# Optimization experiments

Hardware: AMD Instinct MI355X
Metric: run time of the kernel (lower is better)

The kernel has to match this reference:

```python
import jax, jax.numpy as jnp
import numpy as np

EPS = 1e-5

def _layernorm(x, g, b):
    mu = jnp.mean(x, axis=-1, keepdims=True)
    var = jnp.mean((x - mu) ** 2, axis=-1, keepdims=True)
    return (x - mu) / jnp.sqrt(var + EPS) * g + b


def setup_inputs() -> dict:
    key = jax.random.key(0)
    ks = jax.random.split(key, 4)
    B, H, W, C = 8, 96, 96, 256
    return {
        "x1": jax.random.normal(ks[0], (B, H, W, C), dtype=jnp.float32),
        "x2": jax.random.normal(ks[1], (B, H, W, C), dtype=jnp.float32),
        # norm1 (shared LayerNorm applied to both x1 and x2)
        "g1": jnp.ones((C,), jnp.float32),
        "b1": jnp.zeros((C,), jnp.float32),
        # reprojection 1x1 conv: C -> 2C
        "Wr": jax.random.normal(ks[2], (2 * C, C), dtype=jnp.float32) * 0.05,
        "br": jnp.zeros((2 * C,), jnp.float32),
        # final LayerNorm over 2C
        "g2": jnp.ones((2 * C,), jnp.float32),
        "b2": jnp.zeros((2 * C,), jnp.float32),
        # learnable mixing scalars
        "a1": jnp.array(0.25, jnp.float32),
        "a2": jnp.array(0.25, jnp.float32),
        "a3": jnp.array(0.25, jnp.float32),
        "a4": jnp.array(0.25, jnpp_ := jnp.float32),
    }


def reference(x1, x2, g1, b1, Wr, br, g2, b2, a1, a2, a3, a4):
    B, H, W, C = x1.shape
    N, D = H * W, C  # head_count = 1, key_channels = value_channels = D
    n1 = _layernorm(x1.reshape(B, N, C), g1, b1)  # [B,N,D]
    n2 = _layernorm(x2.reshape(B, N, C), g1, b1)

    kq = jnp.swapaxes(n2, 1, 2)                   # [B,D,N]
    key_sm = jax.nn.softmax(kq, axis=2)           # softmax over N
    query = jax.nn.softmax(kq, axis=1)            # softmax over D
    value = jnp.swapaxes(n1, 1, 2)                # [B,D,N]

    # context = key @ value^T : [B,D,D]
    context = jnp.einsum('bdn,ben->bde', key_sm, value)

    def masked_softmax(k):
        # torch.topk + scatter mask == keep entries >= k-th largest per row
        thr = jax.lax.top_k(context, k)[0][..., -1:]
        return jax.nn.softmax(jnp.where(context >= thr, context, -jnp.inf), axis=-1)

    ks = [D // 2, (D * 2) // 3, (D * 3) // 4, (D * 4) // 5]
    o = [jnp.einsum('bde,ben->bdn', masked_softmax(k), query) for k in ks]
    att = a1 * o[0] + a2 * o[1] + a3 * o[2] + a4 * o[3]  # [B,D,N]

    # 1x1 conv reprojection D -> 2D, then LayerNorm over channels
    rep = jnp.einsum('oc,bcn->bno', Wr, att) + br         # [B,N,2D]
    rep = _layernorm(rep, g2, b2)
    # view(B,H,W,2C).permute(0,3,1,2)
    return jnp.transpose(rep.reshape(B, H, W, 2 * C), (0, 3, 1, 2))
```

## Files before the change

### kernel.cpp

```cpp
#include <hip/hip_runtime.h>
#include <hip/hip_bf16.h>

#define Bc 8
#define Nn 9216
#define Dd 256
#define Oo 512
#define EPSc 1e-5f

#define OFF_MU1    0
#define OFF_RSTD1  73728
#define OFF_MU2    147456
#define OFF_RSTD2  221184
#define OFF_ROWINV 294912
#define OFF_COLSUM 368640
#define OFF_M      894976
#define OFF_W2T    1419264
#define OFF_CTXP   2467840

typedef __attribute__((ext_vector_type(4))) float f32x4;
typedef __attribute__((ext_vector_type(8))) short short8;
typedef __attribute__((ext_vector_type(8))) unsigned short ushort8;

static __device__ __forceinline__ unsigned short f2bf(float f) {
    __hip_bfloat16 h = __float2bfloat16(f);
    union { __hip_bfloat16 hh; unsigned short uu; } cv; cv.hh = h;
    return cv.uu;
}

#define SWZ(ch) (((((ch) >> 2) & 7)) ^ ((((ch) & 3)) << 1))

__global__ __launch_bounds__(256) void mg_k0_zero(float* __restrict__ p, int n4) {
    int i = blockIdx.x * 256 + threadIdx.x;
    if (i < n4) ((float4*)p)[i] = make_float4(0.f, 0.f, 0.f, 0.f);
}

__global__ __launch_bounds__(256) void mg_k1_stats(const float* __restrict__ x1, const float* __restrict__ x2,
                                                   const float* __restrict__ g1, const float* __restrict__ b1,
                                                   float* __restrict__ ws)
{
    float* mu1    = ws + OFF_MU1;
    float* rstd1  = ws + OFF_RSTD1;
    float* mu2    = ws + OFF_MU2;
    float* rstd2  = ws + OFF_RSTD2;
    float* rowinv = ws + OFF_ROWINV;
    float* colsum = ws + OFF_COLSUM;

    int t = threadIdx.x, lane = t & 63, w = t >> 6;
    int b = blockIdx.x / 144, rb = blockIdx.x % 144;
    int nbase = rb * 64;

    float4 g1v = ((const float4*)g1)[lane];
    float4 b1v = ((const float4*)b1)[lane];
    float cs0 = 0.f, cs1 = 0.f, cs2 = 0.f, cs3 = 0.f;
    __shared__ float csL[4][256];

    for (int i = 0; i < 16; ++i) {
        int n = nbase + i * 4 + w;
        int base = (b * Nn + n) * 64 + lane;
        float4 xa = ((const float4*)x1)[base];
        float4 xb = ((const float4*)x2)[base];
        float s1 = xa.x + xa.y + xa.z + xa.w;
        float q1 = xa.x*xa.x + xa.y*xa.y + xa.z*xa.z + xa.w*xa.w;
        float s2 = xb.x + xb.y + xb.z + xb.w;
        float q2 = xb.x*xb.x + xb.y*xb.y + xb.z*xb.z + xb.w*xb.w;
        #pragma unroll
        for (int m = 1; m < 64; m <<= 1) {
            s1 += __shfl_xor(s1, m); q1 += __shfl_xor(q1, m);
            s2 += __shfl_xor(s2, m); q2 += __shfl_xor(q2, m);
        }
        float m1 = s1 * (1.f / Dd), m2 = s2 * (1.f / Dd);
        float r1 = rsqrtf(q1 * (1.f / Dd) - m1 * m1 + EPSc);
        float r2 = rsqrtf(q2 * (1.f / Dd) - m2 * m2 + EPSc);
        int ni = b * Nn + n;
        if (lane == 0) { mu1[ni] = m1; rstd1[ni] = r1; mu2[ni] = m2; rstd2[ni] = r2; }
        float e0 = __expf((xb.x - m2) * r2 * g1v.x + b1v.x);
        float e1 = __expf((xb.y - m2) * r2 * g1v.y + b1v.y);
        float e2 = __expf((xb.z - m2) * r2 * g1v.z + b1v.z);
        float e3 = __expf((xb.w - m2) * r2 * g1v.w + b1v.w);
        float rs = e0 + e1 + e2 + e3;
        #pragma unroll
        for (int m = 1; m < 64; m <<= 1) rs += __shfl_xor(rs, m);
        if (lane == 0) rowinv[ni] = 1.f / rs;
        cs0 += e0; cs1 += e1; cs2 += e2; cs3 += e3;
    }
    csL[w][lane * 4 + 0] = cs0;
    csL[w][lane * 4 + 1] = cs1;
    csL[w][lane * 4 + 2] = cs2;
    csL[w][lane * 4 + 3] = cs3;
    __syncthreads();
    float tot = csL[0][t] + csL[1][t] + csL[2][t] + csL[3][t];
    atomicAdd(&colsum[b * Dd + t], tot);
}

__global__ __launch_bounds__(512, 2) void mg_k3_ctx(const float* __restrict__ x1, const float* __restrict__ x2,
                                                    const float* __restrict__ g1, const float* __restrict__ b1,
                                                    float* __restrict__ ws, int nks)
{
    __shared__ ushort PA[256 * 64];
    __shared__ ushort PB[256 * 64];
    const float* mu1   = ws + OFF_MU1;
    const float* rstd1 = ws + OFF_RSTD1;
    const float* mu2   = ws + OFF_MU2;
    const float* rstd2 = ws + OFF_RSTD2;
    float* ctxp = ws + OFF_CTXP;

    int t = threadIdx.x;
    int ks_i = blockIdx.x % nks;
    int b = blockIdx.x / nks;
    int krange = Nn / nks;
    int ntiles = krange >> 6;
    int n_base = ks_i * krange;

    int o  = t >> 6;
    int c4 = t & 63;

    f32x4 g1v = ((const f32x4*)g1)[c4];
    f32x4 b1v = ((const f32x4*)b1)[c4];

    int lane = t & 63, wave = t >> 6;
    int wd = wave & 3, we = wave >> 2;
    int l15 = lane & 15, kgrp = lane >> 4;

    f32x4 acc[4][8];
    #pragma unroll
    for (int dt = 0; dt < 4; ++dt)
        #pragma unroll
        for (int et = 0; et < 8; ++et) acc[dt][et] = (f32x4){0.f, 0.f, 0.f, 0.f};

    for (int st = 0; st < ntiles; ++st) {
        int rowb = b * Nn + n_base + st * 64 + o * 8;
        __syncthreads();
        {
            f32x4 mv0 = *(const f32x4*)(mu1 + rowb),   mv1 = *(const f32x4*)(mu1 + rowb + 4);
            f32x4 rv0 = *(const f32x4*)(rstd1 + rowb), rv1 = *(const f32x4*)(rstd1 + rowb + 4);
            float mva[8] = {mv0[0], mv0[1], mv0[2], mv0[3], mv1[0], mv1[1], mv1[2], mv1[3]};
            float rva[8] = {rv0[0], rv0[1], rv0[2], rv0[3], rv1[0], rv1[1], rv1[2], rv1[3]};
            f32x4 xv[8];
            #pragma unroll
            for (int rr = 0; rr < 8; ++rr)
                xv[rr] = ((const f32x4*)x1)[(size_t)(rowb + rr) * 64 + c4];
            #pragma unroll
            for (int i = 0; i < 4; ++i) {
                int ch = c4 * 4 + i;
                ushort8 u;
                #pragma unroll
                for (int rr = 0; rr < 8; ++rr)
                    u[rr] = f2bf((xv[rr][i] - mva[rr]) * rva[rr] * g1v[i] + b1v[i]);
                *(ushort8*)&PB[ch * 64 + ((o + SWZ(ch)) & 7) * 8] = u;
            }
        }
        {
            f32x4 mv0 = *(const f32x4*)(mu2 + rowb),   mv1 = *(const f32x4*)(mu2 + rowb + 4);
            f32x4 rv0 = *(const f32x4*)(rstd2 + rowb), rv1 = *(const f32x4*)(rstd2 + rowb + 4);
            float mva[8] = {mv0[0], mv0[1], mv0[2], mv0[3], mv1[0], mv1[1], mv1[2], mv1[3]};
            float rva[8] = {rv0[0], rv0[1], rv0[2], rv0[3], rv1[0], rv1[1], rv1[2], rv1[3]};
            f32x4 xv[8];
            #pragma unroll
            for (int rr = 0; rr < 8; ++rr)
                xv[rr] = ((const f32x4*)x2)[(size_t)(rowb + rr) * 64 + c4];
            #pragma unroll
            for (int i = 0; i < 4; ++i) {
                int ch = c4 * 4 + i;
                ushort8 u;
                #pragma unroll
                for (int rr = 0; rr < 8; ++rr)
                    u[rr] = f2bf(__expf((xv[rr][i] - mva[rr]) * rva[rr] * g1v[i] + b1v[i]));
                *(ushort8*)&PA[ch * 64 + ((o + SWZ(ch)) & 7) * 8] = u;
            }
        }
        __syncthreads();

        #pragma unroll
        for (int kk = 0; kk < 2; ++kk) {
            short8 af[4], bf[8];
            #pragma unroll
            for (int dt = 0; dt < 4; ++dt) {
                int ch = wd * 64 + dt * 16 + l15;
                af[dt] = *(const short8*)&PA[ch * 64 + (((kk << 2) + kgrp + SWZ(ch)) & 7) * 8];
            }
            #pragma unroll
            for (int et = 0; et < 8; ++et) {
                int ch = we * 128 + et * 16 + l15;
                bf[et] = *(const short8*)&PB[ch * 64 + (((kk << 2) + kgrp + SWZ(ch)) & 7) * 8];
            }
            #pragma unroll
            for (int dt = 0; dt < 4; ++dt)
                #pragma unroll
                for (int et = 0; et < 8; ++et)
                    acc[dt][et] = __builtin_amdgcn_mfma_f32_16x16x32_bf16(af[dt], bf[et], acc[dt][et], 0, 0, 0);
        }
    }

    size_t obase = ((size_t)ks_i * Bc + b) * (Dd * Dd);
    #pragma unroll
    for (int dt = 0; dt < 4; ++dt) {
        #pragma unroll
        for (int r = 0; r < 4; ++r) {
            int d = wd * 64 + dt * 16 + kgrp * 4 + r;
            float* rowp = ctxp + obase + (size_t)d * Dd + we * 128 + l15;
            #pragma unroll
            for (int et = 0; et < 8; ++et)
                rowp[et * 16] = acc[dt][et][r];
        }
    }
}

__global__ __launch_bounds__(256) void mg_k5_mask(const float* __restrict__ a1p, const float* __restrict__ a2p,
                                                  const float* __restrict__ a3p, const float* __restrict__ a4p,
                                                  float* __restrict__ ws, int nks)
{
    const float* ctxp   = ws + OFF_CTXP;
    const float* colsum = ws + OFF_COLSUM;
    float* Mo = ws + OFF_M;
    int t = threadIdx.x;
    int b = blockIdx.x >> 8, d = blockIdx.x & 255;
    __shared__ float s[256];
    __shared__ float wred[4][4];

    float c = 0.f;
    for (int p = 0; p < nks; ++p)
        c += ctxp[((size_t)p * Bc + b) * (Dd * Dd) + (size_t)d * Dd + t];
    float inv = 1.f / colsum[b * Dd + d];
    c *= inv;
    s[t] = c;
    __syncthreads();
    for (int k = 2; k <= 256; k <<= 1) {
        for (int j = k >> 1; j > 0; j >>= 1) {
            int ixj = t ^ j;
            if (ixj > t) {
                float A = s[t], Bv = s[ixj];
                bool desc = ((t & k) == 0);
                bool sw = desc ? (A < Bv) : (A > Bv);
                if (sw) { s[t] = Bv; s[ixj] = A; }
            }
            __syncthreads();
        }
    }
    float cmax = s[0];
    float t0 = s[127], t1 = s[169], t2 = s[191], t3 = s[203];
    float e = __expf(c - cmax);
    float w0 = (c >= t0) ? e : 0.f;
    float w1 = (c >= t1) ? e : 0.f;
    float w2 = (c >= t2) ? e : 0.f;
    float w3 = (c >= t3) ? e : 0.f;
    float v0 = w0, v1 = w1, v2 = w2, v3 = w3;
    #pragma unroll
    for (int m = 1; m < 64; m <<= 1) {
        v0 += __shfl_xor(v0, m); v1 += __shfl_xor(v1, m);
        v2 += __shfl_xor(v2, m); v3 += __shfl_xor(v3, m);
    }
    int lane = t & 63, wv = t >> 6;
    if (lane == 0) { wred[wv][0] = v0; wred[wv][1] = v1; wred[wv][2] = v2; wred[wv][3] = v3; }
    __syncthreads();
    float S0 = wred[0][0] + wred[1][0] + wred[2][0] + wred[3][0];
    float S1 = wred[0][1] + wred[1][1] + wred[2][1] + wred[3][1];
    float S2 = wred[0][2] + wred[1][2] + wred[2][2] + wred[3][2];
    float S3 = wred[0][3] + wred[1][3] + wred[2][3] + wred[3][3];
    float Mv = a1p[0] * (w0 / S0) + a2p[0] * (w1 / S1) + a3p[0] * (w2 / S2) + a4p[0] * (w3 / S3);
    Mo[(b * Dd + d) * Dd + t] = Mv;
}

__global__ __launch_bounds__(256) void mg_k6_w2(const float* __restrict__ Wr, float* __restrict__ ws)
{
    const float* Mo = ws + OFF_M;
    ushort* W2B = (ushort*)(ws + OFF_W2T);
    __shared__ float Mt[32][128];
    __shared__ float WrT[32][36];
    int t = threadIdx.x;
    int b = blockIdx.x >> 5, ob = (blockIdx.x >> 1) & 15, eh = blockIdx.x & 1;
    int o0 = ob * 32, e0 = eh * 128;
    int ol4 = t & 7, el = t >> 3;
    float acc[4][4];
    #pragma unroll
    for (int i = 0; i < 4; ++i)
        #pragma unroll
        for (int j = 0; j < 4; ++j) acc[i][j] = 0.f;

    for (int ch = 0; ch < 8; ++ch) {
        int c0 = ch * 32;
        __syncthreads();
        #pragma unroll
        for (int k = 0; k < 4; ++k) {
            int fi = t + k * 256;
            int row = fi >> 5, c4 = fi & 31;
            float4 mv = ((const float4*)Mo)[(b * Dd + c0 + row) * 64 + (e0 >> 2) + c4];
            *(float4*)&Mt[row][c4 * 4] = mv;
        }
        {
            int ol = t >> 3, c4 = t & 7;
            float4 wv = ((const float4*)Wr)[(o0 + ol) * 64 + (c0 >> 2) + c4];
            WrT[c4 * 4 + 0][ol] = wv.x;
            WrT[c4 * 4 + 1][ol] = wv.y;
            WrT[c4 * 4 + 2][ol] = wv.z;
            WrT[c4 * 4 + 3][ol] = wv.w;
        }
        __syncthreads();
        #pragma unroll
        for (int cc = 0; cc < 32; ++cc) {
            float4 w4 = *(const float4*)&WrT[cc][ol4 * 4];
            float4 m4 = *(const float4*)&Mt[cc][el * 4];
            float wv[4] = {w4.x, w4.y, w4.z, w4.w};
            float mv[4] = {m4.x, m4.y, m4.z, m4.w};
            #pragma unroll
            for (int i = 0; i < 4; ++i)
                #pragma unroll
                for (int j = 0; j < 4; ++j)
                    acc[i][j] = fmaf(wv[i], mv[j], acc[i][j]);
        }
    }
    #pragma unroll
    for (int i = 0; i < 4; ++i) {
        int o = o0 + ol4 * 4 + i;
        ushort4 u;
        u.x = f2bf(acc[i][0]); u.y = f2bf(acc[i][1]);
        u.z = f2bf(acc[i][2]); u.w = f2bf(acc[i][3]);
        *(ushort4*)&W2B[((size_t)b * Oo + o) * Dd + e0 + el * 4] = u;
    }
}

__global__ __launch_bounds__(256, 3) void mg_k7_final(const float* __restrict__ x2,
        const float* __restrict__ g1, const float* __restrict__ b1,
        const float* __restrict__ br, const float* __restrict__ g2, const float* __restrict__ b2,
        const float* __restrict__ ws, float* __restrict__ out)
{
    __shared__ ushort qsT[32 * 256];
    __shared__ float g1s[256], b1s[256];
    __shared__ float stat[4][2][16][2];
    __shared__ float musig[32][2];

    const float* mu2    = ws + OFF_MU2;
    const float* rstd2  = ws + OFF_RSTD2;
    const float* rowinv = ws + OFF_ROWINV;
    const ushort* W2B   = (const ushort*)(ws + OFF_W2T);

    int t = threadIdx.x;
    int b = blockIdx.x / 288, nt0 = blockIdx.x % 288;
    int n0 = nt0 * 32;
    g1s[t] = g1[t]; b1s[t] = b1[t];
    __syncthreads();

    #pragma unroll
    for (int k = 0; k < 4; ++k) {
        int fi = t + k * 256;
        int row = fi >> 5, g = fi & 31;
        int ni = b * Nn + n0 + row;
        float m = mu2[ni], r = rstd2[ni], ri = rowinv[ni];
        const float4* xp = (const float4*)x2 + (size_t)ni * 64 + g * 2;
        float4 xa = xp[0], xb = xp[1];
        int e = g * 8;
        float v[8] = {xa.x, xa.y, xa.z, xa.w, xb.x, xb.y, xb.z, xb.w};
        ushort8 u;
        #pragma unroll
        for (int j = 0; j < 8; ++j)
            u[j] = f2bf(__expf((v[j] - m) * r * g1s[e + j] + b1s[e + j]) * ri);
        *(ushort8*)&qsT[row * 256 + ((g ^ (row & 7)) << 3)] = u;
    }
    __syncthreads();

    int lw = t & 63, wave = t >> 6;
    int colA = lw & 15, kgrp = lw >> 4;

    f32x4 acc[8][2];
    #pragma unroll
    for (int ot = 0; ot < 8; ++ot) {
        acc[ot][0] = (f32x4){0.f, 0.f, 0.f, 0.f};
        acc[ot][1] = (f32x4){0.f, 0.f, 0.f, 0.f};
    }

    const ushort* abase = W2B + ((size_t)b * Oo + wave * 128 + colA) * Dd + kgrp * 8;

    for (int ks = 0; ks < 8; ++ks) {
        int g = ks * 4 + kgrp;
        int gs = (g ^ (colA & 7)) << 3;
        short8 bf0 = *(const short8*)&qsT[(colA) * 256 + gs];
        short8 bf1 = *(const short8*)&qsT[(16 + colA) * 256 + gs];
        #pragma unroll
        for (int ot = 0; ot < 8; ++ot) {
            short8 af = *(const short8*)&abase[(size_t)ot * 16 * Dd + ks * 32];
            acc[ot][0] = __builtin_amdgcn_mfma_f32_16x16x32_bf16(af, bf0, acc[ot][0], 0, 0, 0);
            acc[ot][1] = __builtin_amdgcn_mfma_f32_16x16x32_bf16(af, bf1, acc[ot][1], 0, 0, 0);
        }
    }

    float ps[2] = {0.f, 0.f}, pq[2] = {0.f, 0.f};
    #pragma unroll
    for (int ot = 0; ot < 8; ++ot) {
        #pragma unroll
        for (int r = 0; r < 4; ++r) {
            int o = wave * 128 + ot * 16 + kgrp * 4 + r;
            float bb = br[o];
            float v0 = acc[ot][0][r] + bb;
            float v1 = acc[ot][1][r] + bb;
            acc[ot][0][r] = v0; acc[ot][1][r] = v1;
            ps[0] += v0; pq[0] += v0 * v0;
            ps[1] += v1; pq[1] += v1 * v1;
        }
    }
    #pragma unroll
    for (int m = 16; m <= 32; m <<= 1) {
        ps[0] += __shfl_xor(ps[0], m); pq[0] += __shfl_xor(pq[0], m);
        ps[1] += __shfl_xor(ps[1], m); pq[1] += __shfl_xor(pq[1], m);
    }
    if (lw < 16) {
        stat[wave][0][lw][0] = ps[0]; stat[wave][0][lw][1] = pq[0];
        stat[wave][1][lw][0] = ps[1]; stat[wave][1][lw][1] = pq[1];
    }
    __syncthreads();
    if (t < 32) {
        int ntile = t >> 4, col = t & 15;
        float S = 0.f, Q = 0.f;
        #pragma unroll
        for (int w2 = 0; w2 < 4; ++w2) { S += stat[w2][ntile][col][0]; Q += stat[w2][ntile][col][1]; }
        float mu = S * (1.f / Oo);
        float var = Q * (1.f / Oo) - mu * mu;
        musig[t][0] = mu;
        musig[t][1] = rsqrtf(var + EPSc);
    }
    __syncthreads();

    float mn0 = musig[colA][0],      rs0 = musig[colA][1];
    float mn1 = musig[16 + colA][0], rs1 = musig[16 + colA][1];
    #pragma unroll
    for (int ot = 0; ot < 8; ++ot) {
        #pragma unroll
        for (int r = 0; r < 4; ++r) {
            int o = wave * 128 + ot * 16 + kgrp * 4 + r;
            float gg = g2[o], bb2 = b2[o];
            size_t ob = ((size_t)b * Oo + o) * Nn + n0;
            out[ob + colA]      = (acc[ot][0][r] - mn0) * rs0 * gg + bb2;
            out[ob + 16 + colA] = (acc[ot][1][r] - mn1) * rs1 * gg + bb2;
        }
    }
}

extern "C" void kernel_launch(void* const* d_in, const int* in_sizes, int n_in,
                              void* d_out, int out_size, void* d_ws, size_t ws_size,
                              hipStream_t stream)
{
    (void)in_sizes; (void)n_in; (void)out_size;
    const float* x1 = (const float*)d_in[0];
    const float* x2 = (const float*)d_in[1];
    const float* g1 = (const float*)d_in[2];
    const float* b1 = (const float*)d_in[3];
    const float* Wr = (const float*)d_in[4];
    const float* br = (const float*)d_in[5];
    const float* g2 = (const float*)d_in[6];
    const float* b2 = (const float*)d_in[7];
    const float* a1 = (const float*)d_in[8];
    const float* a2 = (const float*)d_in[9];
    const float* a3 = (const float*)d_in[10];
    const float* a4 = (const float*)d_in[11];
    float* ws = (float*)d_ws;
    float* out = (float*)d_out;

    const int cand[6] = {24, 16, 12, 8, 4, 2};
    int nks = 2;
    for (int ci = 0; ci < 6; ++ci) {
        if ((2467840ull + (size_t)cand[ci] * 524288ull) * 4ull <= ws_size) { nks = cand[ci]; break; }
    }

    hipLaunchKernelGGL(mg_k0_zero, dim3(2), dim3(256), 0, stream, ws + OFF_COLSUM, 512);
    hipLaunchKernelGGL(mg_k1_stats, dim3(1152), dim3(256), 0, stream, x1, x2, g1, b1, ws);
    hipLaunchKernelGGL(mg_k3_ctx, dim3(Bc * nks), dim3(512), 0, stream, x1, x2, g1, b1, ws, nks);
    hipLaunchKernelGGL(mg_k5_mask, dim3(2048), dim3(256), 0, stream, a1, a2, a3, a4, ws, nks);
    hipLaunchKernelGGL(mg_k6_w2, dim3(256), dim3(256), 0, stream, Wr, ws);
    hipLaunchKernelGGL(mg_k7_final, dim3(2304), dim3(256), 0, stream, x2, g1, b1, br, g2, b2, ws, out);
}
```

Before: 229.4 us.

## Double N-tile width in final GEMM kernel and double-buffer W2 fragment loads

```diff
diff --git a/kernel.cpp b/kernel.cpp
--- a/kernel.cpp
+++ b/kernel.cpp
@@ -318,15 +318,14 @@
     }
 }
 
-__global__ __launch_bounds__(256, 3) void mg_k7_final(const float* __restrict__ x2,
+__global__ __launch_bounds__(256, 2) void mg_k7_final(const float* __restrict__ x2,
         const float* __restrict__ g1, const float* __restrict__ b1,
         const float* __restrict__ br, const float* __restrict__ g2, const float* __restrict__ b2,
         const float* __restrict__ ws, float* __restrict__ out)
 {
-    __shared__ ushort qsT[32 * 256];
-    __shared__ float g1s[256], b1s[256];
-    __shared__ float stat[4][2][16][2];
-    __shared__ float musig[32][2];
+    __shared__ ushort qsT[64 * 256];
+    __shared__ float stat[4][4][16][2];
+    __shared__ float musig[64][2];
 
     const float* mu2    = ws + OFF_MU2;
     const float* rstd2  = ws + OFF_RSTD2;
@@ -334,83 +333,116 @@
     const ushort* W2B   = (const ushort*)(ws + OFF_W2T);
 
     int t = threadIdx.x;
-    int b = blockIdx.x / 288, nt0 = blockIdx.x % 288;
-    int n0 = nt0 * 32;
-    g1s[t] = g1[t]; b1s[t] = b1[t];
-    __syncthreads();
-
-    #pragma unroll
-    for (int k = 0; k < 4; ++k) {
-        int fi = t + k * 256;
-        int row = fi >> 5, g = fi & 31;
+    int b = blockIdx.x / 144, nt0 = blockIdx.x % 144;
+    int n0 = nt0 * 64;
+
+    {
+        int row = t >> 2, gb = (t & 3) * 8;
         int ni = b * Nn + n0 + row;
         float m = mu2[ni], r = rstd2[ni], ri = rowinv[ni];
-        const float4* xp = (const float4*)x2 + (size_t)ni * 64 + g * 2;
-        float4 xa = xp[0], xb = xp[1];
-        int e = g * 8;
-        float v[8] = {xa.x, xa.y, xa.z, xa.w, xb.x, xb.y, xb.z, xb.w};
-        ushort8 u;
-        #pragma unroll
-        for (int j = 0; j < 8; ++j)
-            u[j] = f2bf(__expf((v[j] - m) * r * g1s[e + j] + b1s[e + j]) * ri);
-        *(ushort8*)&qsT[row * 256 + ((g ^ (row & 7)) << 3)] = u;
+        #pragma unroll
+        for (int j = 0; j < 8; ++j) {
+            int g = gb + j;
+            int e = g * 8;
+            const float4* xp = (const float4*)x2 + (size_t)ni * 64 + g * 2;
+            float4 xa = xp[0], xb = xp[1];
+            float4 ga = ((const float4*)g1)[g * 2], gb4 = ((const float4*)g1)[g * 2 + 1];
+            float4 ba = ((const float4*)b1)[g * 2], bb4 = ((const float4*)b1)[g * 2 + 1];
+            float v[8]  = {xa.x, xa.y, xa.z, xa.w, xb.x, xb.y, xb.z, xb.w};
+            float gv[8] = {ga.x, ga.y, ga.z, ga.w, gb4.x, gb4.y, gb4.z, gb4.w};
+            float bv[8] = {ba.x, ba.y, ba.z, ba.w, bb4.x, bb4.y, bb4.z, bb4.w};
+            ushort8 u;
+            #pragma unroll
+            for (int q = 0; q < 8; ++q)
+                u[q] = f2bf(__expf((v[q] - m) * r * gv[q] + bv[q]) * ri);
+            (void)e;
+            *(ushort8*)&qsT[row * 256 + ((g ^ (row & 7)) << 3)] = u;
+        }
     }
     __syncthreads();
 
     int lw = t & 63, wave = t >> 6;
     int colA = lw & 15, kgrp = lw >> 4;
 
-    f32x4 acc[8][2];
-    #pragma unroll
-    for (int ot = 0; ot < 8; ++ot) {
-        acc[ot][0] = (f32x4){0.f, 0.f, 0.f, 0.f};
-        acc[ot][1] = (f32x4){0.f, 0.f, 0.f, 0.f};
-    }
+    f32x4 acc[8][4];
+    #pragma unroll
+    for (int ot = 0; ot < 8; ++ot)
+        #pragma unroll
+        for (int nt = 0; nt < 4; ++nt)
+            acc[ot][nt] = (f32x4){0.f, 0.f, 0.f, 0.f};
 
     const ushort* abase = W2B + ((size_t)b * Oo + wave * 128 + colA) * Dd + kgrp * 8;
 
-    for (int ks = 0; ks < 8; ++ks) {
-        int g = ks * 4 + kgrp;
-        int gs = (g ^ (colA & 7)) << 3;
-        short8 bf0 = *(const short8*)&qsT[(colA) * 256 + gs];
-        short8 bf1 = *(const short8*)&qsT[(16 + colA) * 256 + gs];
-        #pragma unroll
-        for (int ot = 0; ot < 8; ++ot) {
-            short8 af = *(const short8*)&abase[(size_t)ot * 16 * Dd + ks * 32];
-            acc[ot][0] = __builtin_amdgcn_mfma_f32_16x16x32_bf16(af, bf0, acc[ot][0], 0, 0, 0);
-            acc[ot][1] = __builtin_amdgcn_mfma_f32_16x16x32_bf16(af, bf1, acc[ot][1], 0, 0, 0);
-        }
-    }
-
-    float ps[2] = {0.f, 0.f}, pq[2] = {0.f, 0.f};
+#define LOADAF(dst, ksv)                                                        \
+    {                                                                           \
+        _Pragma("unroll")                                                       \
+        for (int ot = 0; ot < 8; ++ot)                                          \
+            dst[ot] = *(const short8*)&abase[(size_t)ot * 16 * Dd + (ksv) * 32];\
+    }
+
+#define MFMASTEP(afv, ksv)                                                      \
+    {                                                                           \
+        short8 bf[4];                                                           \
+        int gsl = (((ksv) * 4 + kgrp) ^ (colA & 7)) << 3;                       \
+        _Pragma("unroll")                                                       \
+        for (int nt = 0; nt < 4; ++nt)                                          \
+            bf[nt] = *(const short8*)&qsT[(nt * 16 + colA) * 256 + gsl];        \
+        _Pragma("unroll")                                                       \
+        for (int ot = 0; ot < 8; ++ot)                                          \
+            _Pragma("unroll")                                                   \
+            for (int nt = 0; nt < 4; ++nt)                                      \
+                acc[ot][nt] = __builtin_amdgcn_mfma_f32_16x16x32_bf16(          \
+                    afv[ot], bf[nt], acc[ot][nt], 0, 0, 0);                     \
+    }
+
+    short8 afA[8], afB[8];
+    LOADAF(afA, 0);
+    #pragma unroll
+    for (int kp = 0; kp < 4; ++kp) {
+        LOADAF(afB, 2 * kp + 1);
+        MFMASTEP(afA, 2 * kp);
+        if (kp < 3) LOADAF(afA, 2 * kp + 2);
+        MFMASTEP(afB, 2 * kp + 1);
+    }
+#undef LOADAF
+#undef MFMASTEP
+
+    float ps[4] = {0.f, 0.f, 0.f, 0.f}, pq[4] = {0.f, 0.f, 0.f, 0.f};
     #pragma unroll
     for (int ot = 0; ot < 8; ++ot) {
         #pragma unroll
         for (int r = 0; r < 4; ++r) {
             int o = wave * 128 + ot * 16 + kgrp * 4 + r;
             float bb = br[o];
-            float v0 = acc[ot][0][r] + bb;
-            float v1 = acc[ot][1][r] + bb;
-            acc[ot][0][r] = v0; acc[ot][1][r] = v1;
-            ps[0] += v0; pq[0] += v0 * v0;
-            ps[1] += v1; pq[1] += v1 * v1;
+            #pragma unroll
+            for (int nt = 0; nt < 4; ++nt) {
+                float v = acc[ot][nt][r] + bb;
+                acc[ot][nt][r] = v;
+                ps[nt] += v; pq[nt] += v * v;
+            }
         }
     }
     #pragma unroll
     for (int m = 16; m <= 32; m <<= 1) {
-        ps[0] += __shfl_xor(ps[0], m); pq[0] += __shfl_xor(pq[0], m);
-        ps[1] += __shfl_xor(ps[1], m); pq[1] += __shfl_xor(pq[1], m);
+        #pragma unroll
+        for (int nt = 0; nt < 4; ++nt) {
+            ps[nt] += __shfl_xor(ps[nt], m);
+            pq[nt] += __shfl_xor(pq[nt], m);
+        }
     }
     if (lw < 16) {
-        stat[wave][0][lw][0] = ps[0]; stat[wave][0][lw][1] = pq[0];
-        stat[wave][1][lw][0] = ps[1]; stat[wave][1][lw][1] = pq[1];
+        #pragma unroll
+        for (int nt = 0; nt < 4; ++nt) {
+            stat[wave][nt][lw][0] = ps[nt];
+            stat[wave][nt][lw][1] = pq[nt];
+        }
     }
     __syncthreads();
-    if (t < 32) {
-        int ntile = t >> 4, col = t & 15;
+    if (t < 64) {
+        int ntl = t >> 4, col = t & 15;
         float S = 0.f, Q = 0.f;
         #pragma unroll
-        for (int w2 = 0; w2 < 4; ++w2) { S += stat[w2][ntile][col][0]; Q += stat[w2][ntile][col][1]; }
+        for (int w2 = 0; w2 < 4; ++w2) { S += stat[w2][ntl][col][0]; Q += stat[w2][ntl][col][1]; }
         float mu = S * (1.f / Oo);
         float var = Q * (1.f / Oo) - mu * mu;
         musig[t][0] = mu;
@@ -418,8 +450,12 @@
     }
     __syncthreads();
 
-    float mn0 = musig[colA][0],      rs0 = musig[colA][1];
-    float mn1 = musig[16 + colA][0], rs1 = musig[16 + colA][1];
+    float mn[4], rs[4];
+    #pragma unroll
+    for (int nt = 0; nt < 4; ++nt) {
+        mn[nt] = musig[nt * 16 + colA][0];
+        rs[nt] = musig[nt * 16 + colA][1];
+    }
     #pragma unroll
     for (int ot = 0; ot < 8; ++ot) {
         #pragma unroll
@@ -427,8 +463,9 @@
             int o = wave * 128 + ot * 16 + kgrp * 4 + r;
             float gg = g2[o], bb2 = b2[o];
             size_t ob = ((size_t)b * Oo + o) * Nn + n0;
-            out[ob + colA]      = (acc[ot][0][r] - mn0) * rs0 * gg + bb2;
-            out[ob + 16 + colA] = (acc[ot][1][r] - mn1) * rs1 * gg + bb2;
+            #pragma unroll
+            for (int nt = 0; nt < 4; ++nt)
+                out[ob + nt * 16 + colA] = (acc[ot][nt][r] - mn[nt]) * rs[nt] * gg + bb2;
         }
     }
 }
@@ -464,5 +501,5 @@
     hipLaunchKernelGGL(mg_k3_ctx, dim3(Bc * nks), dim3(512), 0, stream, x1, x2, g1, b1, ws, nks);
     hipLaunchKernelGGL(mg_k5_mask, dim3(2048), dim3(256), 0, stream, a1, a2, a3, a4, ws, nks);
     hipLaunchKernelGGL(mg_k6_w2, dim3(256), dim3(256), 0, stream, Wr, ws);
-    hipLaunchKernelGGL(mg_k7_final, dim3(2304), dim3(256), 0, stream, x2, g1, b1, br, g2, b2, ws, out);
-}
+    hipLaunchKernelGGL(mg_k7_final, dim3(1152), dim3(256), 0, stream, x2, g1, b1, br, g2, b2, ws, out);
+}
```

Result: faster. 216.8 us (-5.5%).

## Re-layout W2 in k-slab blocks, use 512 threads and double-buffer A loads

Applied to the files above, without the earlier changes.

```diff
diff --git a/kernel.cpp b/kernel.cpp
--- a/kernel.cpp
+++ b/kernel.cpp
@@ -308,24 +308,27 @@
                     acc[i][j] = fmaf(wv[i], mv[j], acc[i][j]);
         }
     }
-    #pragma unroll
-    for (int i = 0; i < 4; ++i) {
-        int o = o0 + ol4 * 4 + i;
-        ushort4 u;
-        u.x = f2bf(acc[i][0]); u.y = f2bf(acc[i][1]);
-        u.z = f2bf(acc[i][2]); u.w = f2bf(acc[i][3]);
-        *(ushort4*)&W2B[((size_t)b * Oo + o) * Dd + e0 + el * 4] = u;
-    }
-}
-
-__global__ __launch_bounds__(256, 3) void mg_k7_final(const float* __restrict__ x2,
+    {
+        int ee = e0 + el * 4;
+        int ks = ee >> 5, eloc = ee & 31;
+        #pragma unroll
+        for (int i = 0; i < 4; ++i) {
+            int o = o0 + ol4 * 4 + i;
+            ushort4 u;
+            u.x = f2bf(acc[i][0]); u.y = f2bf(acc[i][1]);
+            u.z = f2bf(acc[i][2]); u.w = f2bf(acc[i][3]);
+            *(ushort4*)&W2B[(((size_t)b * 8 + ks) * Oo + o) * 32 + eloc] = u;
+        }
+    }
+}
+
+__global__ __launch_bounds__(512) void mg_k7_final(const float* __restrict__ x2,
         const float* __restrict__ g1, const float* __restrict__ b1,
         const float* __restrict__ br, const float* __restrict__ g2, const float* __restrict__ b2,
         const float* __restrict__ ws, float* __restrict__ out)
 {
     __shared__ ushort qsT[32 * 256];
-    __shared__ float g1s[256], b1s[256];
-    __shared__ float stat[4][2][16][2];
+    __shared__ float stat[8][2][16][2];
     __shared__ float musig[32][2];
 
     const float* mu2    = ws + OFF_MU2;
@@ -336,58 +339,81 @@
     int t = threadIdx.x;
     int b = blockIdx.x / 288, nt0 = blockIdx.x % 288;
     int n0 = nt0 * 32;
-    g1s[t] = g1[t]; b1s[t] = b1[t];
-    __syncthreads();
-
-    #pragma unroll
-    for (int k = 0; k < 4; ++k) {
-        int fi = t + k * 256;
-        int row = fi >> 5, g = fi & 31;
+
+    {
+        int row = t >> 4, gb = (t & 15) * 2;
         int ni = b * Nn + n0 + row;
         float m = mu2[ni], r = rstd2[ni], ri = rowinv[ni];
-        const float4* xp = (const float4*)x2 + (size_t)ni * 64 + g * 2;
-        float4 xa = xp[0], xb = xp[1];
-        int e = g * 8;
-        float v[8] = {xa.x, xa.y, xa.z, xa.w, xb.x, xb.y, xb.z, xb.w};
-        ushort8 u;
-        #pragma unroll
-        for (int j = 0; j < 8; ++j)
-            u[j] = f2bf(__expf((v[j] - m) * r * g1s[e + j] + b1s[e + j]) * ri);
-        *(ushort8*)&qsT[row * 256 + ((g ^ (row & 7)) << 3)] = u;
+        #pragma unroll
+        for (int jj = 0; jj < 2; ++jj) {
+            int g = gb + jj;
+            const float4* xp = (const float4*)x2 + (size_t)ni * 64 + g * 2;
+            float4 xa = xp[0], xb = xp[1];
+            float4 ga = ((const float4*)g1)[g * 2], gc = ((const float4*)g1)[g * 2 + 1];
+            float4 ba = ((const float4*)b1)[g * 2], bc = ((const float4*)b1)[g * 2 + 1];
+            float v[8]  = {xa.x, xa.y, xa.z, xa.w, xb.x, xb.y, xb.z, xb.w};
+            float gv[8] = {ga.x, ga.y, ga.z, ga.w, gc.x, gc.y, gc.z, gc.w};
+            float bv[8] = {ba.x, ba.y, ba.z, ba.w, bc.x, bc.y, bc.z, bc.w};
+            ushort8 u;
+            #pragma unroll
+            for (int q = 0; q < 8; ++q)
+                u[q] = f2bf(__expf((v[q] - m) * r * gv[q] + bv[q]) * ri);
+            *(ushort8*)&qsT[row * 256 + ((g ^ (row & 7)) << 3)] = u;
+        }
     }
     __syncthreads();
 
     int lw = t & 63, wave = t >> 6;
     int colA = lw & 15, kgrp = lw >> 4;
 
-    f32x4 acc[8][2];
-    #pragma unroll
-    for (int ot = 0; ot < 8; ++ot) {
+    f32x4 acc[4][2];
+    #pragma unroll
+    for (int ot = 0; ot < 4; ++ot) {
         acc[ot][0] = (f32x4){0.f, 0.f, 0.f, 0.f};
         acc[ot][1] = (f32x4){0.f, 0.f, 0.f, 0.f};
     }
 
-    const ushort* abase = W2B + ((size_t)b * Oo + wave * 128 + colA) * Dd + kgrp * 8;
-
-    for (int ks = 0; ks < 8; ++ks) {
-        int g = ks * 4 + kgrp;
-        int gs = (g ^ (colA & 7)) << 3;
-        short8 bf0 = *(const short8*)&qsT[(colA) * 256 + gs];
-        short8 bf1 = *(const short8*)&qsT[(16 + colA) * 256 + gs];
-        #pragma unroll
-        for (int ot = 0; ot < 8; ++ot) {
-            short8 af = *(const short8*)&abase[(size_t)ot * 16 * Dd + ks * 32];
-            acc[ot][0] = __builtin_amdgcn_mfma_f32_16x16x32_bf16(af, bf0, acc[ot][0], 0, 0, 0);
-            acc[ot][1] = __builtin_amdgcn_mfma_f32_16x16x32_bf16(af, bf1, acc[ot][1], 0, 0, 0);
-        }
-    }
+    const ushort* abase = W2B + ((size_t)b * 8 * Oo + wave * 64 + colA) * 32 + kgrp * 8;
+
+#define LOADAF(dst, ksv)                                                         \
+    {                                                                            \
+        _Pragma("unroll")                                                        \
+        for (int ot = 0; ot < 4; ++ot)                                           \
+            dst[ot] = *(const short8*)&abase[((size_t)(ksv) * Oo + ot * 16) * 32];\
+    }
+
+#define MFMASTEP(afv, ksv)                                                       \
+    {                                                                            \
+        int gsl = (((ksv) * 4 + kgrp) ^ (colA & 7)) << 3;                        \
+        short8 bf0 = *(const short8*)&qsT[colA * 256 + gsl];                     \
+        short8 bf1 = *(const short8*)&qsT[(16 + colA) * 256 + gsl];              \
+        _Pragma("unroll")                                                        \
+        for (int ot = 0; ot < 4; ++ot) {                                         \
+            acc[ot][0] = __builtin_amdgcn_mfma_f32_16x16x32_bf16(                \
+                afv[ot], bf0, acc[ot][0], 0, 0, 0);                              \
+            acc[ot][1] = __builtin_amdgcn_mfma_f32_16x16x32_bf16(                \
+                afv[ot], bf1, acc[ot][1], 0, 0, 0);                              \
+        }                                                                        \
+    }
+
+    short8 afA[4], afB[4];
+    LOADAF(afA, 0);
+    #pragma unroll
+    for (int kp = 0; kp < 4; ++kp) {
+        LOADAF(afB, 2 * kp + 1);
+        MFMASTEP(afA, 2 * kp);
+        if (kp < 3) LOADAF(afA, 2 * kp + 2);
+        MFMASTEP(afB, 2 * kp + 1);
+    }
+#undef LOADAF
+#undef MFMASTEP
 
     float ps[2] = {0.f, 0.f}, pq[2] = {0.f, 0.f};
     #pragma unroll
-    for (int ot = 0; ot < 8; ++ot) {
+    for (int ot = 0; ot < 4; ++ot) {
         #pragma unroll
         for (int r = 0; r < 4; ++r) {
-            int o = wave * 128 + ot * 16 + kgrp * 4 + r;
+            int o = wave * 64 + ot * 16 + kgrp * 4 + r;
             float bb = br[o];
             float v0 = acc[ot][0][r] + bb;
             float v1 = acc[ot][1][r] + bb;
@@ -407,10 +433,10 @@
     }
     __syncthreads();
     if (t < 32) {
-        int ntile = t >> 4, col = t & 15;
+        int ntl = t >> 4, col = t & 15;
         float S = 0.f, Q = 0.f;
         #pragma unroll
-        for (int w2 = 0; w2 < 4; ++w2) { S += stat[w2][ntile][col][0]; Q += stat[w2][ntile][col][1]; }
+        for (int w2 = 0; w2 < 8; ++w2) { S += stat[w2][ntl][col][0]; Q += stat[w2][ntl][col][1]; }
         float mu = S * (1.f / Oo);
         float var = Q * (1.f / Oo) - mu * mu;
         musig[t][0] = mu;
@@ -421,10 +447,10 @@
     float mn0 = musig[colA][0],      rs0 = musig[colA][1];
     float mn1 = musig[16 + colA][0], rs1 = musig[16 + colA][1];
     #pragma unroll
-    for (int ot = 0; ot < 8; ++ot) {
+    for (int ot = 0; ot < 4; ++ot) {
         #pragma unroll
         for (int r = 0; r < 4; ++r) {
-            int o = wave * 128 + ot * 16 + kgrp * 4 + r;
+            int o = wave * 64 + ot * 16 + kgrp * 4 + r;
             float gg = g2[o], bb2 = b2[o];
             size_t ob = ((size_t)b * Oo + o) * Nn + n0;
             out[ob + colA]      = (acc[ot][0][r] - mn0) * rs0 * gg + bb2;
@@ -464,5 +490,5 @@
     hipLaunchKernelGGL(mg_k3_ctx, dim3(Bc * nks), dim3(512), 0, stream, x1, x2, g1, b1, ws, nks);
     hipLaunchKernelGGL(mg_k5_mask, dim3(2048), dim3(256), 0, stream, a1, a2, a3, a4, ws, nks);
     hipLaunchKernelGGL(mg_k6_w2, dim3(256), dim3(256), 0, stream, Wr, ws);
-    hipLaunchKernelGGL(mg_k7_final, dim3(2304), dim3(256), 0, stream, x2, g1, b1, br, g2, b2, ws, out);
-}
+    hipLaunchKernelGGL(mg_k7_final, dim3(2304), dim3(512), 0, stream, x2, g1, b1, br, g2, b2, ws, out);
+}
```

Result: faster. 200.9 us (-12.4%).
